# Performance work log

Measured on AMD Instinct MI355X. Metric: run time of the kernel, lower is better.

Reference implementation:

```python
import jax, jax.numpy as jnp
import numpy as np

NEG_SLOPE = 0.2  # PyG GATConv default leaky_relu slope
BN_EPS = 1e-5


def gat_conv(x_src, x_dst, src, dst, w_src, w_dst, att_src, att_dst, bias):
    """Bipartite PyG GATConv, heads=H, concat=False (mean over heads), add_self_loops=True.
    x_src: [Ns, F], x_dst: [Nd, F]; src/dst: [E] int edge index; w_*: [F, H*C]; att_*: [H, C]; bias: [C].
    """
    H, C = att_src.shape
    n_dst = x_dst.shape[0]
    hs = (x_src @ w_src).reshape(-1, H, C)            # [Ns, H, C]
    hd = (x_dst @ w_dst).reshape(-1, H, C)            # [Nd, H, C]
    a_s = (hs * att_src[None]).sum(-1)                # [Ns, H]
    a_d = (hd * att_dst[None]).sum(-1)                # [Nd, H]
    # PyG adds self loops with num_nodes = min(Ns, Nd) for bipartite inputs
    n_loop = min(x_src.shape[0], n_dst)
    loop = jnp.arange(n_loop, dtype=src.dtype)
    src = jnp.concatenate([src, loop])
    dst = jnp.concatenate([dst, loop])
    e = jax.nn.leaky_relu(a_s[src] + a_d[dst], NEG_SLOPE)           # [E+L, H]
    m = jax.ops.segment_max(e, dst, num_segments=n_dst)             # [Nd, H]
    ex = jnp.exp(e - m[dst])
    den = jax.ops.segment_sum(ex, dst, num_segments=n_dst)
    alpha = ex / (den[dst] + 1e-16)                                 # neighborhood softmax
    msg = hs[src] * alpha[:, :, None]                               # [E+L, H, C]
    out = jax.ops.segment_sum(msg, dst, num_segments=n_dst)         # [Nd, H, C]
    return out.mean(axis=1) + bias


def _forward(user_ids, ingredient_ids, recipe_x, ing_src, ing_dst, ub_src, ub_dst,
             user_table, ing_table, W_rl, b_rl, bn_gamma, bn_beta,
             g1_ws, g1_wd, g1_as, g1_ad, g1_b,
             g2_ws, g2_wd, g2_as, g2_ad, g2_b):
    # nn.Embedding(max_norm=1.0): renorm looked-up rows to L2 norm <= 1
    u = user_table[user_ids]
    un = jnp.linalg.norm(u, axis=-1, keepdims=True)
    u = u * jnp.where(un > 1.0, 1.0 / (un + 1e-7), 1.0)
    # static ingredient embedding lookup
    ing = ing_table[ingredient_ids]
    # recipe linear + BatchNorm (training-mode batch stats; dropout off = eval)
    r = recipe_x @ W_rl + b_rl
    mu = r.mean(axis=0)
    var = ((r - mu) ** 2).mean(axis=0)
    r = bn_gamma * (r - mu) * jax.lax.rsqrt(var + BN_EPS) + bn_beta
    # ingredient -> recipe GAT, residual add
    r = r + gat_conv(ing, r, ing_src, ing_dst, g1_ws, g1_wd, g1_as, g1_ad, g1_b)
    # user -> recipe GAT
    r = gat_conv(u, r, ub_src, ub_dst, g2_ws, g2_wd, g2_as, g2_ad, g2_b)
    return r


def setup_inputs() -> dict:
    key = jax.random.key(0)
    ks = jax.random.split(key, 24)
    NU, NR, NI = 50000, 100000, 20000
    D_IN, H, C = 20, 2, 128
    E1, E2 = 400000, 800000
    s = 0.05
    f32 = jnp.float32
    inp = {
        "user_ids": jax.random.randint(ks[0], (NU,), 0, NU, dtype=jnp.int32),
        "ingredient_ids": jax.random.randint(ks[1], (NI,), 0, NI, dtype=jnp.int32),
        "recipe_x": jax.random.normal(ks[2], (NR, D_IN), f32),
        "ing_src": jax.random.randint(ks[3], (E1,), 0, NI, dtype=jnp.int32),
        "ing_dst": jax.random.randint(ks[4], (E1,), 0, NR, dtype=jnp.int32),
        "ub_src": jax.random.randint(ks[5], (E2,), 0, NU, dtype=jnp.int32),
        "ub_dst": jax.random.randint(ks[6], (E2,), 0, NR, dtype=jnp.int32),
        "user_table": jax.random.normal(ks[7], (NU, C), f32) * s,
        "ing_table": jax.random.normal(ks[8], (NI, C), f32) * s,
        "W_rl": jax.random.normal(ks[9], (D_IN, C), f32) * s,
        "b_rl": jnp.zeros((C,), f32),
        "bn_gamma": jnp.ones((C,), f32),
        "bn_beta": jnp.zeros((C,), f32),
        "g1_ws": jax.random.normal(ks[10], (C, H * C), f32) * s,
        "g1_wd": jax.random.normal(ks[11], (C, H * C), f32) * s,
        "g1_as": jax.random.normal(ks[12], (H, C), f32) * s,
        "g1_ad": jax.random.normal(ks[13], (H, C), f32) * s,
        "g1_b": jnp.zeros((C,), f32),
        "g2_ws": jax.random.normal(ks[14], (C, H * C), f32) * s,
        "g2_wd": jax.random.normal(ks[15], (C, H * C), f32) * s,
        "g2_as": jax.random.normal(ks[16], (H, C), f32) * s,
        "g2_ad": jax.random.normal(ks[17], (H, C), f32) * s,
        "g2_b": jnp.zeros((C,), f32),
    }
    return inp


def reference(user_ids, ingredient_ids, recipe_x, ing_src, ing_dst, ub_src, ub_dst,
              user_table, ing_table, W_rl, b_rl, bn_gamma, bn_beta,
              g1_ws, g1_wd, g1_as, g1_ad, g1_b,
              g2_ws, g2_wd, g2_as, g2_ad, g2_b):
    return _forward(user_ids, ingredient_ids, recipe_x, ing_src, ing_dst, ub_src, ub_dst,
                    user_table, ing_table, W_rl, b_rl, bn_gamma, bn_beta,
                    g1_ws, g1_wd, g1_as, g1_ad, g1_b,
                    g2_ws, g2_wd, g2_as, g2_ad, g2_b)
```

## Files before the change

### kernel.cpp

```cpp
#include <hip/hip_runtime.h>
#include <hip/hip_bf16.h>
#include <math.h>

#define DIN 20
#define C 128
#define HC 256
#define EB1 8192
#define EB2 2048
#define MAXNB 400

typedef unsigned short u16;
typedef unsigned int u32;
typedef unsigned long long u64;
typedef __bf16 bf16x8 __attribute__((ext_vector_type(8)));
typedef float f32x4 __attribute__((ext_vector_type(4)));

__device__ __forceinline__ float bfbits2f(unsigned int lo16) {
    return __uint_as_float(lo16 << 16);
}
__device__ __forceinline__ u16 f2bf_rne(float f) {
    unsigned int b = __float_as_uint(f);
    return (u16)((b + 0x7FFFu + ((b >> 16) & 1u)) >> 16);
}

__device__ __forceinline__ void scan512f(u32* cnt, u32* off, u32* wsum4) {
    int t = threadIdx.x;
    int l = t & 63, w = t >> 6;
    u32 a = cnt[2 * t], b = cnt[2 * t + 1];
    u32 s = a + b;
    u32 isc = s;
    #pragma unroll
    for (int o = 1; o < 64; o <<= 1) {
        u32 n = __shfl_up(isc, o);
        if (l >= o) isc += n;
    }
    if (l == 63) wsum4[w] = isc;
    __syncthreads();
    u32 pre = 0;
    if (w > 0) pre += wsum4[0];
    if (w > 1) pre += wsum4[1];
    if (w > 2) pre += wsum4[2];
    u32 excl = pre + isc - s;
    off[2 * t] = excl;
    off[2 * t + 1] = excl + a;
    __syncthreads();
}

__device__ __forceinline__ void edge_at(int i, const int* s1, const int* d1,
    const int* s2, const int* d2, int E1, int T1, int E2, int NR,
    int& s, int& key)
{
    if (i < T1) {
        if (i < E1) { s = s1[i]; key = d1[i]; }
        else        { s = i - E1; key = i - E1; }
    } else {
        int k = i - T1;
        if (k < E2) { s = s2[k]; key = NR + d2[k]; }
        else        { s = k - E2; key = NR + (k - E2); }
    }
}

__global__ __launch_bounds__(256) void k_init(const float* __restrict__ x, int NR,
    float* __restrict__ stats, int SB,
    const int* __restrict__ src1, const int* __restrict__ dst1,
    const int* __restrict__ src2, const int* __restrict__ dst2,
    int E1, int L1, int E2, int L2, int NB, u32* __restrict__ bucketCnt)
{
    __shared__ float L[256][DIN];
    __shared__ u32 cnt[MAXNB];
    int t = threadIdx.x;
    if (blockIdx.x < SB) {
        int r = blockIdx.x * 256 + t;
        if (r < NR) {
            #pragma unroll
            for (int k = 0; k < DIN; k++) L[t][k] = x[r * DIN + k];
        } else {
            #pragma unroll
            for (int k = 0; k < DIN; k++) L[t][k] = 0.f;
        }
        __syncthreads();
        if (t < 210) {
            int p = 0, q = t;
            while (q >= DIN - p) { q -= (DIN - p); p++; }
            q += p;
            float acc = 0.f;
            for (int rr = 0; rr < 256; rr++) acc += L[rr][p] * L[rr][q];
            atomicAdd(&stats[p * DIN + q], acc);
            if (p != q) atomicAdd(&stats[q * DIN + p], acc);
        } else if (t < 230) {
            int k = t - 210;
            float acc = 0.f;
            for (int rr = 0; rr < 256; rr++) acc += L[rr][k];
            atomicAdd(&stats[400 + k], acc);
        }
        return;
    }
    for (int i = t; i < NB; i += 256) cnt[i] = 0;
    __syncthreads();
    int T1 = E1 + L1, T = T1 + E2 + L2;
    int base = (blockIdx.x - SB) * EB1;
    int nE = T - base; if (nE > EB1) nE = EB1;
    for (int j = t; j < nE; j += 256) {
        int s, key;
        edge_at(base + j, src1, dst1, src2, dst2, E1, T1, E2, NR, s, key);
        atomicAdd(&cnt[key >> 9], 1u);
    }
    __syncthreads();
    for (int b = t; b < NB; b += 256) {
        u32 c = cnt[b];
        if (c) atomicAdd(&bucketCnt[b], c);
    }
}

__global__ __launch_bounds__(256) void k_precomp_pack(float* __restrict__ stats,
    const float* __restrict__ W,
    const float* __restrict__ gamma, const float* __restrict__ beta,
    const float* __restrict__ g1_wd, const float* __restrict__ g1_ad,
    const float* __restrict__ g2_wd, const float* __restrict__ g2_ad,
    const float* __restrict__ g1_ws, const float* __restrict__ g1_as,
    const float* __restrict__ g2_ws, const float* __restrict__ g2_as,
    const float* __restrict__ g1b, float invN, u16* __restrict__ wsp,
    const u32* __restrict__ bucketCnt, int NB, int n2,
    u32* __restrict__ bucketBase, u32* __restrict__ gcur, int* __restrict__ off)
{
    int t = threadIdx.x;
    if (blockIdx.x == 33) {
        __shared__ u32 cnt[512], offL[512], wsum4[4];
        for (int i = t; i < 512; i += 256) cnt[i] = (i < NB) ? bucketCnt[i] : 0u;
        __syncthreads();
        scan512f(cnt, offL, wsum4);
        for (int i = t; i < NB; i += 256) {
            u32 v = offL[i];
            bucketBase[i] = v;
            gcur[i] = v;
        }
        if (t == 0) {
            u32 total = offL[511] + cnt[511];
            bucketBase[NB] = total;
            off[n2] = (int)total;
        }
        return;
    }
    if (blockIdx.x > 0) {
        int idx0 = ((blockIdx.x - 1) * 256 + t) * 4;
        #pragma unroll
        for (int i = 0; i < 4; i++) {
            int flat = idx0 + i;
            int j = flat & 7;
            int lane = (flat >> 3) & 63;
            int kb = (flat >> 9) & 3;
            int nt = flat >> 11;
            int k = kb * 32 + (lane >> 4) * 8 + j;
            int n = nt * 16 + (lane & 15);
            wsp[flat] = f2bf_rne(g2_ws[k * HC + n]);
        }
        return;
    }
    __shared__ float Sm[420];
    __shared__ float Wm[DIN * C];
    __shared__ float vd1s[256];
    __shared__ float vd2s[256];
    __shared__ float sS[128];
    __shared__ float sSh[128];
    for (int i = t; i < 420; i += 256) Sm[i] = stats[i];
    for (int i = t; i < DIN * C; i += 256) Wm[i] = W[i];
    __syncthreads();
    if (t < C) {
        float w[DIN];
        #pragma unroll
        for (int k = 0; k < DIN; k++) w[k] = Wm[k * C + t];
        float mb = 0.f;
        #pragma unroll
        for (int k = 0; k < DIN; k++) mb += Sm[400 + k] * invN * w[k];
        float e2 = 0.f;
        for (int p = 0; p < DIN; p++) {
            float acc2 = 0.f;
            #pragma unroll
            for (int q = 0; q < DIN; q++) acc2 += Sm[p * DIN + q] * w[q];
            e2 += w[p] * acc2;
        }
        e2 *= invN;
        float var = e2 - mb * mb;
        float s = gamma[t] * rsqrtf(var + 1e-5f);
        float sh = beta[t] - s * mb;
        stats[420 + t] = s;
        stats[548 + t] = sh;
        sS[t] = s;
        sSh[t] = sh;
    }
    {
        int k = t >> 1, h = t & 1;
        const float4* wd1 = (const float4*)(g1_wd + k * HC + h * C);
        const float4* wd2 = (const float4*)(g2_wd + k * HC + h * C);
        const float4* ws1 = (const float4*)(g1_ws + k * HC + h * C);
        const float4* ws2 = (const float4*)(g2_ws + k * HC + h * C);
        const float4* ad1 = (const float4*)(g1_ad + h * C);
        const float4* ad2 = (const float4*)(g2_ad + h * C);
        const float4* as1 = (const float4*)(g1_as + h * C);
        const float4* as2 = (const float4*)(g2_as + h * C);
        float a1 = 0.f, a2 = 0.f, s1 = 0.f, s2 = 0.f;
        #pragma unroll 4
        for (int q = 0; q < 32; q++) {
            float4 x, y;
            x = wd1[q]; y = ad1[q];
            a1 += x.x * y.x + x.y * y.y + x.z * y.z + x.w * y.w;
            x = wd2[q]; y = ad2[q];
            a2 += x.x * y.x + x.y * y.y + x.z * y.z + x.w * y.w;
            x = ws1[q]; y = as1[q];
            s1 += x.x * y.x + x.y * y.y + x.z * y.z + x.w * y.w;
            x = ws2[q]; y = as2[q];
            s2 += x.x * y.x + x.y * y.y + x.z * y.z + x.w * y.w;
        }
        stats[676 + t] = a1;
        stats[932 + t] = a2;
        stats[1200 + t] = s1;
        stats[1456 + t] = s2;
        vd1s[t] = a1;
        vd2s[t] = a2;
    }
    __syncthreads();
    {
        int k = t >> 1, h = t & 1;
        const float4* ws1p = (const float4*)(g1_ws + k * HC + h * C);
        float t0 = 0.f, t1 = 0.f;
        #pragma unroll 4
        for (int q = 0; q < 32; q++) {
            float4 wv = ws1p[q];
            int c = q * 4;
            t0 += wv.x * vd2s[(c + 0) * 2 + 0] + wv.y * vd2s[(c + 1) * 2 + 0]
                + wv.z * vd2s[(c + 2) * 2 + 0] + wv.w * vd2s[(c + 3) * 2 + 0];
            t1 += wv.x * vd2s[(c + 0) * 2 + 1] + wv.y * vd2s[(c + 1) * 2 + 1]
                + wv.z * vd2s[(c + 2) * 2 + 1] + wv.w * vd2s[(c + 3) * 2 + 1];
        }
        stats[1712 + t * 2 + 0] = t0;
        stats[1712 + t * 2 + 1] = t1;
    }
    if (t < 2) {
        float cb = 0.f;
        for (int k = 0; k < C; k++) cb += g1b[k] * vd2s[k * 2 + t];
        stats[1188 + t] = cb;
    }
    if (t < 80) {
        int k = t >> 2, h4 = t & 3, h = h4 & 1;
        const float* vs = (h4 < 2) ? vd1s : vd2s;
        float acc = 0.f;
        for (int c = 0; c < C; c++) acc += sS[c] * Wm[k * C + c] * vs[c * 2 + h];
        stats[2240 + t] = acc;
    } else if (t < 84) {
        int h4 = t - 80, h = h4 & 1;
        const float* vs = (h4 < 2) ? vd1s : vd2s;
        float acc = 0.f;
        for (int c = 0; c < C; c++) acc += sSh[c] * vs[c * 2 + h];
        stats[2320 + h4] = acc;
    }
}

__global__ __launch_bounds__(256) void k_feat(
    const float* __restrict__ x, int NR, int R0B, int IB,
    const float* __restrict__ ing_table, const int* __restrict__ ing_ids, int NI,
    const float* __restrict__ user_table, const int* __restrict__ user_ids, int NU,
    const u16* __restrict__ wsp, const float* __restrict__ stats,
    float* __restrict__ a_d, float* __restrict__ advd,
    float* __restrict__ a_si, float* __restrict__ psi,
    u16* __restrict__ hs16, float* __restrict__ a_su)
{
    __shared__ float fv[84];
    __shared__ float u1s[256];
    __shared__ float Ts[512];
    __shared__ __align__(16) u16 A[32 * 136];
    __shared__ float u2s[256];
    int t = threadIdx.x;
    int bid = blockIdx.x;
    if (bid < R0B) {
        if (t < 84) fv[t] = stats[2240 + t];
        __syncthreads();
        int r = bid * 256 + t;
        if (r < NR) {
            const float4* xp = (const float4*)(x + (size_t)r * DIN);
            float4 v0 = xp[0], v1 = xp[1], v2 = xp[2], v3 = xp[3], v4 = xp[4];
            float xv[20] = {v0.x, v0.y, v0.z, v0.w, v1.x, v1.y, v1.z, v1.w,
                            v2.x, v2.y, v2.z, v2.w, v3.x, v3.y, v3.z, v3.w,
                            v4.x, v4.y, v4.z, v4.w};
            float a0 = 0.f, a1 = 0.f, b0 = 0.f, b1 = 0.f;
            #pragma unroll
            for (int k = 0; k < DIN; k++) {
                float xvk = xv[k];
                a0 += xvk * fv[k * 4 + 0];
                a1 += xvk * fv[k * 4 + 1];
                b0 += xvk * fv[k * 4 + 2];
                b1 += xvk * fv[k * 4 + 3];
            }
            ((float2*)a_d)[r]  = make_float2(a0 + fv[80], a1 + fv[81]);
            ((float2*)advd)[r] = make_float2(b0 + fv[82], b1 + fv[83]);
        }
        return;
    }
    if (bid < R0B + IB) {
        u1s[t] = stats[1200 + t];
        Ts[t] = stats[1712 + t];
        Ts[256 + t] = stats[1968 + t];
        __syncthreads();
        int r = t >> 3, cg = t & 7;
        int row = (bid - R0B) * 32 + r;
        float as0 = 0.f, as1 = 0.f, p00 = 0.f, p01 = 0.f, p10 = 0.f, p11 = 0.f;
        if (row < NI) {
            const float* xp = ing_table + (size_t)ing_ids[row] * C + cg * 16;
            #pragma unroll
            for (int q = 0; q < 4; q++) {
                float4 v = ((const float4*)xp)[q];
                float xvv[4] = {v.x, v.y, v.z, v.w};
                #pragma unroll
                for (int jj = 0; jj < 4; jj++) {
                    int k = cg * 16 + q * 4 + jj;
                    float xx = xvv[jj];
                    as0 += xx * u1s[k * 2 + 0];
                    as1 += xx * u1s[k * 2 + 1];
                    p00 += xx * Ts[k * 4 + 0];
                    p01 += xx * Ts[k * 4 + 1];
                    p10 += xx * Ts[k * 4 + 2];
                    p11 += xx * Ts[k * 4 + 3];
                }
            }
        }
        #pragma unroll
        for (int m = 1; m <= 4; m <<= 1) {
            as0 += __shfl_xor(as0, m); as1 += __shfl_xor(as1, m);
            p00 += __shfl_xor(p00, m); p01 += __shfl_xor(p01, m);
            p10 += __shfl_xor(p10, m); p11 += __shfl_xor(p11, m);
        }
        if (cg == 0 && row < NI) {
            ((float2*)a_si)[row] = make_float2(as0, as1);
            float4 pv; pv.x = p00; pv.y = p01; pv.z = p10; pv.w = p11;
            ((float4*)psi)[row] = pv;
        }
        return;
    }
    u2s[t] = stats[1456 + t];
    int rowBase = (bid - R0B - IB) * 32;
    int r = t >> 3, cg = t & 7;
    int row = rowBase + r;
    float xv[16];
    if (row < NU) {
        const float* xp = user_table + (size_t)user_ids[row] * C + cg * 16;
        #pragma unroll
        for (int q = 0; q < 4; q++) {
            float4 v = ((const float4*)xp)[q];
            xv[q * 4 + 0] = v.x; xv[q * 4 + 1] = v.y;
            xv[q * 4 + 2] = v.z; xv[q * 4 + 3] = v.w;
        }
    } else {
        #pragma unroll
        for (int q = 0; q < 16; q++) xv[q] = 0.f;
    }
    float ss = 0.f;
    #pragma unroll
    for (int q = 0; q < 16; q++) ss += xv[q] * xv[q];
    #pragma unroll
    for (int m = 1; m <= 4; m <<= 1) ss += __shfl_xor(ss, m);
    float nn = sqrtf(ss);
    float f = (nn > 1.f) ? 1.f / (nn + 1e-7f) : 1.f;
    float as0 = 0.f, as1 = 0.f;
    #pragma unroll
    for (int q = 0; q < 16; q++) {
        xv[q] *= f;
        int k = cg * 16 + q;
        as0 += xv[q] * u2s[k * 2 + 0];
        as1 += xv[q] * u2s[k * 2 + 1];
    }
    #pragma unroll
    for (int m = 1; m <= 4; m <<= 1) {
        as0 += __shfl_xor(as0, m); as1 += __shfl_xor(as1, m);
    }
    if (cg == 0 && row < NU) ((float2*)a_su)[row] = make_float2(as0, as1);
    {
        union { u16 h[16]; uint4 u4[2]; } pk;
        #pragma unroll
        for (int q = 0; q < 16; q++) pk.h[q] = f2bf_rne(xv[q]);
        uint4* dst = (uint4*)&A[r * 136 + cg * 16];
        dst[0] = pk.u4[0];
        dst[1] = pk.u4[1];
    }
    __syncthreads();
    int w = t >> 6, l = t & 63;
    int m15 = l & 15, q4 = l >> 4;
    bf16x8 afrag[2][4];
    #pragma unroll
    for (int mt = 0; mt < 2; mt++)
        #pragma unroll
        for (int kb = 0; kb < 4; kb++)
            afrag[mt][kb] = *(const bf16x8*)&A[(mt * 16 + m15) * 136 + kb * 32 + q4 * 8];
    f32x4 acc[2][4];
    #pragma unroll
    for (int mt = 0; mt < 2; mt++)
        #pragma unroll
        for (int i = 0; i < 4; i++) acc[mt][i] = (f32x4){0.f, 0.f, 0.f, 0.f};
    #pragma unroll
    for (int kb = 0; kb < 4; kb++) {
        #pragma unroll
        for (int i = 0; i < 4; i++) {
            int nt = w * 4 + i;
            bf16x8 bfrag = *(const bf16x8*)&wsp[((nt * 4 + kb) * 64 + l) * 8];
            acc[0][i] = __builtin_amdgcn_mfma_f32_16x16x32_bf16(afrag[0][kb], bfrag, acc[0][i], 0, 0, 0);
            acc[1][i] = __builtin_amdgcn_mfma_f32_16x16x32_bf16(afrag[1][kb], bfrag, acc[1][i], 0, 0, 0);
        }
    }
    #pragma unroll
    for (int mt = 0; mt < 2; mt++) {
        #pragma unroll
        for (int i = 0; i < 4; i++) {
            int col = (w * 4 + i) * 16 + m15;
            #pragma unroll
            for (int rr = 0; rr < 4; rr++) {
                int rw = rowBase + mt * 16 + q4 * 4 + rr;
                if (rw < NU) hs16[(size_t)rw * HC + col] = f2bf_rne(acc[mt][i][rr]);
            }
        }
    }
}

__global__ __launch_bounds__(256) void kA2(const int* __restrict__ src1, const int* __restrict__ dst1,
    const int* __restrict__ src2, const int* __restrict__ dst2,
    int E1, int L1, int E2, int L2, int NR, int NB,
    u32* __restrict__ gcur, u64* __restrict__ pairs)
{
    __shared__ u64 ldsE[EB2];
    __shared__ u64 ldsS[EB2];
    __shared__ u32 cntA[512], cntB[512], offL[512], wsum4[4];
    __shared__ u32 gbase[MAXNB];
    int t = threadIdx.x;
    for (int i = t; i < 512; i += 256) { cntA[i] = 0; cntB[i] = 0; }
    __syncthreads();
    int T1 = E1 + L1, T = T1 + E2 + L2;
    int base = blockIdx.x * EB2;
    int nE = T - base; if (nE > EB2) nE = EB2;
    for (int j = t; j < nE; j += 256) {
        int s, key;
        edge_at(base + j, src1, dst1, src2, dst2, E1, T1, E2, NR, s, key);
        ldsE[j] = ((u64)(u32)key << 32) | (u32)s;
        atomicAdd(&cntA[key >> 9], 1u);
    }
    __syncthreads();
    scan512f(cntA, offL, wsum4);
    for (int b = t; b < NB; b += 256) {
        u32 c = cntA[b];
        gbase[b] = c ? atomicAdd(&gcur[b], c) : 0u;
    }
    __syncthreads();
    for (int j = t; j < nE; j += 256) {
        u64 e = ldsE[j];
        u32 b = ((u32)(e >> 32)) >> 9;
        u32 r = atomicAdd(&cntB[b], 1u);
        ldsS[offL[b] + r] = e;
    }
    __syncthreads();
    for (int j = t; j < nE; j += 256) {
        u64 e = ldsS[j];
        u32 b = ((u32)(e >> 32)) >> 9;
        pairs[gbase[b] + ((u32)j - offL[b])] = e;
    }
}

__global__ __launch_bounds__(256) void kB(const u64* __restrict__ pairs,
    const u32* __restrict__ bucketBase, int n2,
    int* __restrict__ off, int* __restrict__ sorted)
{
    __shared__ u32 cntA[512], cntB[512], offL[512], wsum4[4];
    __shared__ u32 ldsS[8192];
    int b = blockIdx.x;
    int t = threadIdx.x;
    u32 beg = bucketBase[b], end = bucketBase[b + 1];
    int dstBase = b << 9;
    for (int i = t; i < 512; i += 256) { cntA[i] = 0; cntB[i] = 0; }
    __syncthreads();
    for (u32 j = beg + t; j < end; j += 256) {
        u32 key = (u32)(pairs[j] >> 32);
        atomicAdd(&cntA[key - dstBase], 1u);
    }
    __syncthreads();
    scan512f(cntA, offL, wsum4);
    for (int d = t; d < 512; d += 256) {
        int gk = dstBase + d;
        if (gk < n2) off[gk] = (int)(beg + offL[d]);
    }
    u32 cnt = end - beg;
    bool fast = cnt <= 8192u;
    __syncthreads();
    for (u32 j = beg + t; j < end; j += 256) {
        u64 e = pairs[j];
        u32 d = (u32)(e >> 32) - dstBase;
        u32 r = atomicAdd(&cntB[d], 1u);
        u32 pos = offL[d] + r;
        if (fast) ldsS[pos] = (u32)e;
        else sorted[beg + pos] = (int)(u32)e;
    }
    __syncthreads();
    if (fast) {
        for (u32 j = t; j < cnt; j += 256) sorted[beg + j] = (int)ldsS[j];
    }
}

__global__ __launch_bounds__(256) void k_agg(const int* __restrict__ off, const int* __restrict__ sorted,
    const float* __restrict__ a_si, const float* __restrict__ psi,
    const float* __restrict__ a_d1, const float* __restrict__ advd,
    const float* __restrict__ cb,
    const float* __restrict__ a_su, const u16* __restrict__ hs16,
    const float* __restrict__ bias, int NR, float* __restrict__ out)
{
    int wave = threadIdx.x >> 6, lane = threadIdx.x & 63;
    int d = blockIdx.x * 4 + wave;
    if (d >= NR) return;
    int beg = off[d], end = off[d + 1];
    float ad0 = a_d1[d * 2 + 0], ad1 = a_d1[d * 2 + 1];
    float w0s = 0.f, w1s = 0.f, a00 = 0.f, a01 = 0.f, a10 = 0.f, a11 = 0.f;
    for (int j = beg + lane; j < end; j += 64) {
        int s = sorted[j];
        float2 as = ((const float2*)a_si)[s];
        float e0 = as.x + ad0; e0 = (e0 >= 0.f) ? e0 : 0.2f * e0;
        float e1 = as.y + ad1; e1 = (e1 >= 0.f) ? e1 : 0.2f * e1;
        float x0 = __expf(e0), x1 = __expf(e1);
        float4 p = ((const float4*)psi)[s];
        w0s += x0; w1s += x1;
        a00 += x0 * p.x; a01 += x0 * p.y;
        a10 += x1 * p.z; a11 += x1 * p.w;
    }
    #pragma unroll
    for (int o = 1; o < 64; o <<= 1) {
        w0s += __shfl_xor(w0s, o); w1s += __shfl_xor(w1s, o);
        a00 += __shfl_xor(a00, o); a01 += __shfl_xor(a01, o);
        a10 += __shfl_xor(a10, o); a11 += __shfl_xor(a11, o);
    }
    float inv0g = 1.f / (w0s + 1e-16f), inv1g = 1.f / (w1s + 1e-16f);
    float r0 = advd[d * 2 + 0] + cb[0] + 0.5f * (a00 * inv0g + a10 * inv1g);
    float r1 = advd[d * 2 + 1] + cb[1] + 0.5f * (a01 * inv0g + a11 * inv1g);
    int beg2 = off[NR + d], end2 = off[NR + d + 1];
    int head = lane >> 5;
    int q = lane & 31;
    u32 laneoff = (u32)(head * 256 + q * 8);
    int hsel = lane & 32;
    float adh = head ? r1 : r0;
    float wsum = 0.f;
    float acc0 = 0.f, acc1 = 0.f, acc2 = 0.f, acc3 = 0.f;
    const char* hbase = (const char*)hs16;

    for (int base = beg2; base < end2; base += 32) {
        int rem = end2 - base; if (rem > 32) rem = 32;
        int j = q; if (j >= rem) j = rem - 1;
        int sp = sorted[base + j];
        u32 boff = ((u32)sp) << 9;
        float asv = a_su[sp * 2 + head];
        float ee = asv + adh; ee = (ee >= 0.f) ? ee : 0.2f * ee;
        float wcomb = __expf(ee);
        int e = 0;
        for (; e + 4 <= rem; e += 4) {
            u32 b0 = __shfl(boff, e + 0), b1 = __shfl(boff, e + 1);
            u32 b2 = __shfl(boff, e + 2), b3 = __shfl(boff, e + 3);
            uint2 g0 = *(const uint2*)(hbase + (b0 + laneoff));
            uint2 g1 = *(const uint2*)(hbase + (b1 + laneoff));
            uint2 g2 = *(const uint2*)(hbase + (b2 + laneoff));
            uint2 g3 = *(const uint2*)(hbase + (b3 + laneoff));
            float W0 = __shfl(wcomb, hsel + e + 0);
            float W1 = __shfl(wcomb, hsel + e + 1);
            float W2 = __shfl(wcomb, hsel + e + 2);
            float W3 = __shfl(wcomb, hsel + e + 3);
            wsum += (W0 + W1) + (W2 + W3);
            acc0 += W0 * bfbits2f(g0.x & 0xFFFFu);
            acc1 += W0 * __uint_as_float(g0.x & 0xFFFF0000u);
            acc2 += W0 * bfbits2f(g0.y & 0xFFFFu);
            acc3 += W0 * __uint_as_float(g0.y & 0xFFFF0000u);
            acc0 += W1 * bfbits2f(g1.x & 0xFFFFu);
            acc1 += W1 * __uint_as_float(g1.x & 0xFFFF0000u);
            acc2 += W1 * bfbits2f(g1.y & 0xFFFFu);
            acc3 += W1 * __uint_as_float(g1.y & 0xFFFF0000u);
            acc0 += W2 * bfbits2f(g2.x & 0xFFFFu);
            acc1 += W2 * __uint_as_float(g2.x & 0xFFFF0000u);
            acc2 += W2 * bfbits2f(g2.y & 0xFFFFu);
            acc3 += W2 * __uint_as_float(g2.y & 0xFFFF0000u);
            acc0 += W3 * bfbits2f(g3.x & 0xFFFFu);
            acc1 += W3 * __uint_as_float(g3.x & 0xFFFF0000u);
            acc2 += W3 * bfbits2f(g3.y & 0xFFFFu);
            acc3 += W3 * __uint_as_float(g3.y & 0xFFFF0000u);
        }
        for (; e < rem; e++) {
            u32 b0 = __shfl(boff, e);
            float W = __shfl(wcomb, hsel + e);
            uint2 g = *(const uint2*)(hbase + (b0 + laneoff));
            wsum += W;
            acc0 += W * bfbits2f(g.x & 0xFFFFu);
            acc1 += W * __uint_as_float(g.x & 0xFFFF0000u);
            acc2 += W * bfbits2f(g.y & 0xFFFFu);
            acc3 += W * __uint_as_float(g.y & 0xFFFF0000u);
        }
    }
    float inv = 1.f / (wsum + 1e-16f);
    float v0 = acc0 * inv, v1 = acc1 * inv, v2 = acc2 * inv, v3 = acc3 * inv;
    v0 = 0.5f * (v0 + __shfl_xor(v0, 32));
    v1 = 0.5f * (v1 + __shfl_xor(v1, 32));
    v2 = 0.5f * (v2 + __shfl_xor(v2, 32));
    v3 = 0.5f * (v3 + __shfl_xor(v3, 32));
    if (lane < 32) {
        float4 bb = ((const float4*)bias)[q];
        float4 o;
        o.x = v0 + bb.x; o.y = v1 + bb.y; o.z = v2 + bb.z; o.w = v3 + bb.w;
        ((float4*)(out + (size_t)d * C))[q] = o;
    }
}

extern "C" void kernel_launch(void* const* d_in, const int* in_sizes, int n_in,
                              void* d_out, int out_size, void* d_ws, size_t ws_size,
                              hipStream_t stream) {
    const int*   user_ids       = (const int*)d_in[0];
    const int*   ingredient_ids = (const int*)d_in[1];
    const float* recipe_x       = (const float*)d_in[2];
    const int*   ing_src        = (const int*)d_in[3];
    const int*   ing_dst        = (const int*)d_in[4];
    const int*   ub_src         = (const int*)d_in[5];
    const int*   ub_dst         = (const int*)d_in[6];
    const float* user_table     = (const float*)d_in[7];
    const float* ing_table      = (const float*)d_in[8];
    const float* W_rl           = (const float*)d_in[9];
    const float* bn_gamma       = (const float*)d_in[11];
    const float* bn_beta        = (const float*)d_in[12];
    const float* g1_ws          = (const float*)d_in[13];
    const float* g1_wd          = (const float*)d_in[14];
    const float* g1_as          = (const float*)d_in[15];
    const float* g1_ad          = (const float*)d_in[16];
    const float* g1_b           = (const float*)d_in[17];
    const float* g2_ws          = (const float*)d_in[18];
    const float* g2_wd          = (const float*)d_in[19];
    const float* g2_as          = (const float*)d_in[20];
    const float* g2_ad          = (const float*)d_in[21];
    const float* g2_b           = (const float*)d_in[22];

    int NU = in_sizes[0];
    int NI = in_sizes[1];
    int NR = in_sizes[2] / DIN;
    int E1 = in_sizes[3];
    int E2 = in_sizes[5];
    int Nmax = (NI > NU) ? NI : NU;
    int L1 = (NI < NR) ? NI : NR;
    int L2 = (NU < NR) ? NU : NR;
    int Etot = E1 + L1 + E2 + L2;
    int n2 = 2 * NR;
    int NB = (n2 + 511) >> 9;

    char* w = (char*)d_ws;
    u16*   hs16  = (u16*)w;    w += (size_t)Nmax * HC * 2;
    float* a_si  = (float*)w;  w += (size_t)NI * 2 * 4;
    float* a_su  = (float*)w;  w += (size_t)NU * 2 * 4;
    float* psi   = (float*)w;  w += (size_t)NI * 4 * 4;
    float* a_d   = (float*)w;  w += (size_t)NR * 2 * 4;
    float* advd  = (float*)w;  w += (size_t)NR * 2 * 4;
    float* stats = (float*)w;  w += 2432 * 4;
    u32*   bucketCnt  = (u32*)w; w += MAXNB * 4;
    u16*   wsp   = (u16*)w;    w += 32768 * 2;
    u32*   bucketBase = (u32*)w; w += (MAXNB + 1) * 4;
    u32*   gcur  = (u32*)w;    w += MAXNB * 4;
    int*   off   = (int*)w;    w += (size_t)(n2 + 1) * 4;
    int*   sorted= (int*)w;    w += (size_t)Etot * 4;
    w = (char*)(((size_t)w + 15) & ~(size_t)15);
    u64*   pairs = (u64*)w;    w += (size_t)Etot * 8;

    hipMemsetAsync(stats, 0, (2432 + MAXNB) * 4, stream);

    int SB = (NR + 255) / 256;
    int AB = (Etot + EB1 - 1) / EB1;
    k_init<<<SB + AB, 256, 0, stream>>>(recipe_x, NR, stats, SB,
                                        ing_src, ing_dst, ub_src, ub_dst,
                                        E1, L1, E2, L2, NB, bucketCnt);
    k_precomp_pack<<<34, 256, 0, stream>>>(stats, W_rl, bn_gamma, bn_beta,
                                           g1_wd, g1_ad, g2_wd, g2_ad,
                                           g1_ws, g1_as, g2_ws, g2_as, g1_b,
                                           1.0f / NR, wsp,
                                           bucketCnt, NB, n2, bucketBase, gcur, off);
    kA2<<<(Etot + EB2 - 1) / EB2, 256, 0, stream>>>(ing_src, ing_dst, ub_src, ub_dst,
                                                    E1, L1, E2, L2, NR, NB, gcur, pairs);
    int R0B = (NR + 255) / 256;
    int IB  = (NI + 31) / 32;
    int HB  = (NU + 31) / 32;
    k_feat<<<R0B + IB + HB, 256, 0, stream>>>(recipe_x, NR, R0B, IB,
                                              ing_table, ingredient_ids, NI,
                                              user_table, user_ids, NU,
                                              wsp, stats, a_d, advd, a_si, psi,
                                              hs16, a_su);
    kB<<<NB, 256, 0, stream>>>(pairs, bucketBase, n2, off, sorted);
    k_agg<<<(NR + 3) / 4, 256, 0, stream>>>(off, sorted, a_si, psi, a_d, advd,
                                            stats + 1188, a_su, hs16, g2_b, NR,
                                            (float*)d_out);
}
```

Baseline: 352.4 us.

## Merge bucket-sort and feature kernels into fewer launches with shared LDS

Folds the bf16 weight packing into k_init and the edge scatter (kA2) into the feature kernel as k_mid. It also merges the per-bucket sort (kB) with the user GEMM blocks as k_fin, cutting the launch count from six to five. Independent work now runs concurrently inside one grid. To make the merged kernels fit, the scatter chunk EB2 is halved and the LDS fast-path threshold in the bucket sort drops from 8192 to 6144. That sends more buckets down the slower global-scatter path and doubles the number of scatter blocks and global atomics on gcur.

```diff
diff --git a/kernel.cpp b/kernel.cpp
--- a/kernel.cpp
+++ b/kernel.cpp
@@ -6,7 +6,7 @@
 #define C 128
 #define HC 256
 #define EB1 8192
-#define EB2 2048
+#define EB2 1024
 #define MAXNB 400
 
 typedef unsigned short u16;
@@ -61,16 +61,17 @@
 }
 
 __global__ __launch_bounds__(256) void k_init(const float* __restrict__ x, int NR,
-    float* __restrict__ stats, int SB,
-    const int* __restrict__ src1, const int* __restrict__ dst1,
-    const int* __restrict__ src2, const int* __restrict__ dst2,
-    int E1, int L1, int E2, int L2, int NB, u32* __restrict__ bucketCnt)
+    float* __restrict__ stats, int SB, int AB,
+    const int* __restrict__ dst1, const int* __restrict__ dst2,
+    int E1, int L1, int E2, int L2, int NB, u32* __restrict__ bucketCnt,
+    const float* __restrict__ g2_ws, u16* __restrict__ wsp)
 {
     __shared__ float L[256][DIN];
     __shared__ u32 cnt[MAXNB];
     int t = threadIdx.x;
-    if (blockIdx.x < SB) {
-        int r = blockIdx.x * 256 + t;
+    int bid = blockIdx.x;
+    if (bid < SB) {
+        int r = bid * 256 + t;
         if (r < NR) {
             #pragma unroll
             for (int k = 0; k < DIN; k++) L[t][k] = x[r * DIN + k];
@@ -95,36 +96,52 @@
         }
         return;
     }
-    for (int i = t; i < NB; i += 256) cnt[i] = 0;
-    __syncthreads();
-    int T1 = E1 + L1, T = T1 + E2 + L2;
-    int base = (blockIdx.x - SB) * EB1;
-    int nE = T - base; if (nE > EB1) nE = EB1;
-    for (int j = t; j < nE; j += 256) {
-        int s, key;
-        edge_at(base + j, src1, dst1, src2, dst2, E1, T1, E2, NR, s, key);
-        atomicAdd(&cnt[key >> 9], 1u);
-    }
-    __syncthreads();
-    for (int b = t; b < NB; b += 256) {
-        u32 c = cnt[b];
-        if (c) atomicAdd(&bucketCnt[b], c);
-    }
-}
-
-__global__ __launch_bounds__(256) void k_precomp_pack(float* __restrict__ stats,
+    if (bid < SB + AB) {
+        for (int i = t; i < NB; i += 256) cnt[i] = 0;
+        __syncthreads();
+        int T1 = E1 + L1, T = T1 + E2 + L2;
+        int base = (bid - SB) * EB1;
+        int nE = T - base; if (nE > EB1) nE = EB1;
+        for (int j = t; j < nE; j += 256) {
+            int i = base + j, key;
+            if (i < T1) key = (i < E1) ? dst1[i] : (i - E1);
+            else { int k = i - T1; key = NR + ((k < E2) ? dst2[k] : (k - E2)); }
+            atomicAdd(&cnt[key >> 9], 1u);
+        }
+        __syncthreads();
+        for (int b = t; b < NB; b += 256) {
+            u32 c = cnt[b];
+            if (c) atomicAdd(&bucketCnt[b], c);
+        }
+        return;
+    }
+    int idx0 = ((bid - SB - AB) * 256 + t) * 4;
+    #pragma unroll
+    for (int i = 0; i < 4; i++) {
+        int flat = idx0 + i;
+        int j = flat & 7;
+        int lane = (flat >> 3) & 63;
+        int kb = (flat >> 9) & 3;
+        int nt = flat >> 11;
+        int k = kb * 32 + (lane >> 4) * 8 + j;
+        int n = nt * 16 + (lane & 15);
+        wsp[flat] = f2bf_rne(g2_ws[k * HC + n]);
+    }
+}
+
+__global__ __launch_bounds__(256) void k_scanpre(float* __restrict__ stats,
     const float* __restrict__ W,
     const float* __restrict__ gamma, const float* __restrict__ beta,
     const float* __restrict__ g1_wd, const float* __restrict__ g1_ad,
     const float* __restrict__ g2_wd, const float* __restrict__ g2_ad,
     const float* __restrict__ g1_ws, const float* __restrict__ g1_as,
     const float* __restrict__ g2_ws, const float* __restrict__ g2_as,
-    const float* __restrict__ g1b, float invN, u16* __restrict__ wsp,
+    const float* __restrict__ g1b, float invN,
     const u32* __restrict__ bucketCnt, int NB, int n2,
     u32* __restrict__ bucketBase, u32* __restrict__ gcur, int* __restrict__ off)
 {
     int t = threadIdx.x;
-    if (blockIdx.x == 33) {
+    if (blockIdx.x == 1) {
         __shared__ u32 cnt[512], offL[512], wsum4[4];
         for (int i = t; i < 512; i += 256) cnt[i] = (i < NB) ? bucketCnt[i] : 0u;
         __syncthreads();
@@ -138,21 +155,6 @@
             u32 total = offL[511] + cnt[511];
             bucketBase[NB] = total;
             off[n2] = (int)total;
-        }
-        return;
-    }
-    if (blockIdx.x > 0) {
-        int idx0 = ((blockIdx.x - 1) * 256 + t) * 4;
-        #pragma unroll
-        for (int i = 0; i < 4; i++) {
-            int flat = idx0 + i;
-            int j = flat & 7;
-            int lane = (flat >> 3) & 63;
-            int kb = (flat >> 9) & 3;
-            int nt = flat >> 11;
-            int k = kb * 32 + (lane >> 4) * 8 + j;
-            int n = nt * 16 + (lane & 15);
-            wsp[flat] = f2bf_rne(g2_ws[k * HC + n]);
         }
         return;
     }
@@ -255,26 +257,64 @@
     }
 }
 
-__global__ __launch_bounds__(256) void k_feat(
-    const float* __restrict__ x, int NR, int R0B, int IB,
+__global__ __launch_bounds__(256) void k_mid(
+    const int* __restrict__ src1, const int* __restrict__ dst1,
+    const int* __restrict__ src2, const int* __restrict__ dst2,
+    int E1, int L1, int E2, int L2, int NR, int NB,
+    u32* __restrict__ gcur, u64* __restrict__ pairs, int A2B, int R0B,
+    const float* __restrict__ x, const float* __restrict__ stats,
+    float* __restrict__ a_d, float* __restrict__ advd,
     const float* __restrict__ ing_table, const int* __restrict__ ing_ids, int NI,
-    const float* __restrict__ user_table, const int* __restrict__ user_ids, int NU,
-    const u16* __restrict__ wsp, const float* __restrict__ stats,
-    float* __restrict__ a_d, float* __restrict__ advd,
-    float* __restrict__ a_si, float* __restrict__ psi,
-    u16* __restrict__ hs16, float* __restrict__ a_su)
+    float* __restrict__ a_si, float* __restrict__ psi)
 {
-    __shared__ float fv[84];
-    __shared__ float u1s[256];
-    __shared__ float Ts[512];
-    __shared__ __align__(16) u16 A[32 * 136];
-    __shared__ float u2s[256];
+    __shared__ __align__(16) char sm[24144];
     int t = threadIdx.x;
     int bid = blockIdx.x;
-    if (bid < R0B) {
+    if (bid < A2B) {
+        u64* ldsE = (u64*)sm;
+        u64* ldsS = ldsE + EB2;
+        u32* cntA = (u32*)(ldsS + EB2);
+        u32* cntB = cntA + 512;
+        u32* offL = cntB + 512;
+        u32* wsum4 = offL + 512;
+        u32* gbase = wsum4 + 4;
+        for (int i = t; i < 512; i += 256) { cntA[i] = 0; cntB[i] = 0; }
+        __syncthreads();
+        int T1 = E1 + L1, T = T1 + E2 + L2;
+        int base = bid * EB2;
+        int nE = T - base; if (nE > EB2) nE = EB2;
+        for (int j = t; j < nE; j += 256) {
+            int s, key;
+            edge_at(base + j, src1, dst1, src2, dst2, E1, T1, E2, NR, s, key);
+            ldsE[j] = ((u64)(u32)key << 32) | (u32)s;
+            atomicAdd(&cntA[key >> 9], 1u);
+        }
+        __syncthreads();
+        scan512f(cntA, offL, wsum4);
+        for (int b = t; b < NB; b += 256) {
+            u32 c = cntA[b];
+            gbase[b] = c ? atomicAdd(&gcur[b], c) : 0u;
+        }
+        __syncthreads();
+        for (int j = t; j < nE; j += 256) {
+            u64 e = ldsE[j];
+            u32 b = ((u32)(e >> 32)) >> 9;
+            u32 r = atomicAdd(&cntB[b], 1u);
+            ldsS[offL[b] + r] = e;
+        }
+        __syncthreads();
+        for (int j = t; j < nE; j += 256) {
+            u64 e = ldsS[j];
+            u32 b = ((u32)(e >> 32)) >> 9;
+            pairs[gbase[b] + ((u32)j - offL[b])] = e;
+        }
+        return;
+    }
+    if (bid < A2B + R0B) {
+        float* fv = (float*)sm;
         if (t < 84) fv[t] = stats[2240 + t];
         __syncthreads();
-        int r = bid * 256 + t;
+        int r = (bid - A2B) * 256 + t;
         if (r < NR) {
             const float4* xp = (const float4*)(x + (size_t)r * DIN);
             float4 v0 = xp[0], v1 = xp[1], v2 = xp[2], v3 = xp[3], v4 = xp[4];
@@ -295,48 +335,99 @@
         }
         return;
     }
-    if (bid < R0B + IB) {
-        u1s[t] = stats[1200 + t];
-        Ts[t] = stats[1712 + t];
-        Ts[256 + t] = stats[1968 + t];
-        __syncthreads();
-        int r = t >> 3, cg = t & 7;
-        int row = (bid - R0B) * 32 + r;
-        float as0 = 0.f, as1 = 0.f, p00 = 0.f, p01 = 0.f, p10 = 0.f, p11 = 0.f;
-        if (row < NI) {
-            const float* xp = ing_table + (size_t)ing_ids[row] * C + cg * 16;
+    float* u1s = (float*)sm;
+    float* Ts  = u1s + 256;
+    u1s[t] = stats[1200 + t];
+    Ts[t] = stats[1712 + t];
+    Ts[256 + t] = stats[1968 + t];
+    __syncthreads();
+    int r = t >> 3, cg = t & 7;
+    int row = (bid - A2B - R0B) * 32 + r;
+    float as0 = 0.f, as1 = 0.f, p00 = 0.f, p01 = 0.f, p10 = 0.f, p11 = 0.f;
+    if (row < NI) {
+        const float* xp = ing_table + (size_t)ing_ids[row] * C + cg * 16;
+        #pragma unroll
+        for (int q = 0; q < 4; q++) {
+            float4 v = ((const float4*)xp)[q];
+            float xvv[4] = {v.x, v.y, v.z, v.w};
             #pragma unroll
-            for (int q = 0; q < 4; q++) {
-                float4 v = ((const float4*)xp)[q];
-                float xvv[4] = {v.x, v.y, v.z, v.w};
-                #pragma unroll
-                for (int jj = 0; jj < 4; jj++) {
-                    int k = cg * 16 + q * 4 + jj;
-                    float xx = xvv[jj];
-                    as0 += xx * u1s[k * 2 + 0];
-                    as1 += xx * u1s[k * 2 + 1];
-                    p00 += xx * Ts[k * 4 + 0];
-                    p01 += xx * Ts[k * 4 + 1];
-                    p10 += xx * Ts[k * 4 + 2];
-                    p11 += xx * Ts[k * 4 + 3];
-                }
+            for (int jj = 0; jj < 4; jj++) {
+                int k = cg * 16 + q * 4 + jj;
+                float xx = xvv[jj];
+                as0 += xx * u1s[k * 2 + 0];
+                as1 += xx * u1s[k * 2 + 1];
+                p00 += xx * Ts[k * 4 + 0];
+                p01 += xx * Ts[k * 4 + 1];
+                p10 += xx * Ts[k * 4 + 2];
+                p11 += xx * Ts[k * 4 + 3];
             }
         }
-        #pragma unroll
-        for (int m = 1; m <= 4; m <<= 1) {
-            as0 += __shfl_xor(as0, m); as1 += __shfl_xor(as1, m);
-            p00 += __shfl_xor(p00, m); p01 += __shfl_xor(p01, m);
-            p10 += __shfl_xor(p10, m); p11 += __shfl_xor(p11, m);
-        }
-        if (cg == 0 && row < NI) {
-            ((float2*)a_si)[row] = make_float2(as0, as1);
-            float4 pv; pv.x = p00; pv.y = p01; pv.z = p10; pv.w = p11;
-            ((float4*)psi)[row] = pv;
+    }
+    #pragma unroll
+    for (int m = 1; m <= 4; m <<= 1) {
+        as0 += __shfl_xor(as0, m); as1 += __shfl_xor(as1, m);
+        p00 += __shfl_xor(p00, m); p01 += __shfl_xor(p01, m);
+        p10 += __shfl_xor(p10, m); p11 += __shfl_xor(p11, m);
+    }
+    if (cg == 0 && row < NI) {
+        ((float2*)a_si)[row] = make_float2(as0, as1);
+        float4 pv; pv.x = p00; pv.y = p01; pv.z = p10; pv.w = p11;
+        ((float4*)psi)[row] = pv;
+    }
+}
+
+__global__ __launch_bounds__(256) void k_fin(const u64* __restrict__ pairs,
+    const u32* __restrict__ bucketBase, int n2, int NB,
+    int* __restrict__ off, int* __restrict__ sorted,
+    const float* __restrict__ user_table, const int* __restrict__ user_ids, int NU,
+    const u16* __restrict__ wsp, const float* __restrict__ stats,
+    u16* __restrict__ hs16, float* __restrict__ a_su)
+{
+    __shared__ __align__(16) char sm[30736];
+    int t = threadIdx.x;
+    int bid = blockIdx.x;
+    if (bid < NB) {
+        u32* cntA = (u32*)sm;
+        u32* cntB = cntA + 512;
+        u32* offL = cntB + 512;
+        u32* wsum4 = offL + 512;
+        u32* ldsS = wsum4 + 4;
+        int b = bid;
+        u32 beg = bucketBase[b], end = bucketBase[b + 1];
+        int dstBase = b << 9;
+        for (int i = t; i < 512; i += 256) { cntA[i] = 0; cntB[i] = 0; }
+        __syncthreads();
+        for (u32 j = beg + t; j < end; j += 256) {
+            u32 key = (u32)(pairs[j] >> 32);
+            atomicAdd(&cntA[key - dstBase], 1u);
+        }
+        __syncthreads();
+        scan512f(cntA, offL, wsum4);
+        for (int d = t; d < 512; d += 256) {
+            int gk = dstBase + d;
+            if (gk < n2) off[gk] = (int)(beg + offL[d]);
+        }
+        u32 cnt = end - beg;
+        bool fast = cnt <= 6144u;
+        __syncthreads();
+        for (u32 j = beg + t; j < end; j += 256) {
+            u64 e = pairs[j];
+            u32 d = (u32)(e >> 32) - dstBase;
+            u32 r = atomicAdd(&cntB[d], 1u);
+            u32 pos = offL[d] + r;
+            if (fast) ldsS[pos] = (u32)e;
+            else sorted[beg + pos] = (int)(u32)e;
+        }
+        __syncthreads();
+        if (fast) {
+            for (u32 j = t; j < cnt; j += 256) sorted[beg + j] = (int)ldsS[j];
         }
         return;
     }
+    u16* A = (u16*)sm;
+    float* u2s = (float*)(sm + 8704);
     u2s[t] = stats[1456 + t];
-    int rowBase = (bid - R0B - IB) * 32;
+    int rowBase = (bid - NB) * 32;
     int r = t >> 3, cg = t & 7;
     int row = rowBase + r;
     float xv[16];
@@ -415,87 +506,6 @@
                 if (rw < NU) hs16[(size_t)rw * HC + col] = f2bf_rne(acc[mt][i][rr]);
             }
         }
-    }
-}
-
-__global__ __launch_bounds__(256) void kA2(const int* __restrict__ src1, const int* __restrict__ dst1,
-    const int* __restrict__ src2, const int* __restrict__ dst2,
-    int E1, int L1, int E2, int L2, int NR, int NB,
-    u32* __restrict__ gcur, u64* __restrict__ pairs)
-{
-    __shared__ u64 ldsE[EB2];
-    __shared__ u64 ldsS[EB2];
-    __shared__ u32 cntA[512], cntB[512], offL[512], wsum4[4];
-    __shared__ u32 gbase[MAXNB];
-    int t = threadIdx.x;
-    for (int i = t; i < 512; i += 256) { cntA[i] = 0; cntB[i] = 0; }
-    __syncthreads();
-    int T1 = E1 + L1, T = T1 + E2 + L2;
-    int base = blockIdx.x * EB2;
-    int nE = T - base; if (nE > EB2) nE = EB2;
-    for (int j = t; j < nE; j += 256) {
-        int s, key;
-        edge_at(base + j, src1, dst1, src2, dst2, E1, T1, E2, NR, s, key);
-        ldsE[j] = ((u64)(u32)key << 32) | (u32)s;
-        atomicAdd(&cntA[key >> 9], 1u);
-    }
-    __syncthreads();
-    scan512f(cntA, offL, wsum4);
-    for (int b = t; b < NB; b += 256) {
-        u32 c = cntA[b];
-        gbase[b] = c ? atomicAdd(&gcur[b], c) : 0u;
-    }
-    __syncthreads();
-    for (int j = t; j < nE; j += 256) {
-        u64 e = ldsE[j];
-        u32 b = ((u32)(e >> 32)) >> 9;
-        u32 r = atomicAdd(&cntB[b], 1u);
-        ldsS[offL[b] + r] = e;
-    }
-    __syncthreads();
-    for (int j = t; j < nE; j += 256) {
-        u64 e = ldsS[j];
-        u32 b = ((u32)(e >> 32)) >> 9;
-        pairs[gbase[b] + ((u32)j - offL[b])] = e;
-    }
-}
-
-__global__ __launch_bounds__(256) void kB(const u64* __restrict__ pairs,
-    const u32* __restrict__ bucketBase, int n2,
-    int* __restrict__ off, int* __restrict__ sorted)
-{
-    __shared__ u32 cntA[512], cntB[512], offL[512], wsum4[4];
-    __shared__ u32 ldsS[8192];
-    int b = blockIdx.x;
-    int t = threadIdx.x;
-    u32 beg = bucketBase[b], end = bucketBase[b + 1];
-    int dstBase = b << 9;
-    for (int i = t; i < 512; i += 256) { cntA[i] = 0; cntB[i] = 0; }
-    __syncthreads();
-    for (u32 j = beg + t; j < end; j += 256) {
-        u32 key = (u32)(pairs[j] >> 32);
-        atomicAdd(&cntA[key - dstBase], 1u);
-    }
-    __syncthreads();
-    scan512f(cntA, offL, wsum4);
-    for (int d = t; d < 512; d += 256) {
-        int gk = dstBase + d;
-        if (gk < n2) off[gk] = (int)(beg + offL[d]);
-    }
-    u32 cnt = end - beg;
-    bool fast = cnt <= 8192u;
-    __syncthreads();
-    for (u32 j = beg + t; j < end; j += 256) {
-        u64 e = pairs[j];
-        u32 d = (u32)(e >> 32) - dstBase;
-        u32 r = atomicAdd(&cntB[d], 1u);
-        u32 pos = offL[d] + r;
-        if (fast) ldsS[pos] = (u32)e;
-        else sorted[beg + pos] = (int)(u32)e;
-    }
-    __syncthreads();
-    if (fast) {
-        for (u32 j = t; j < cnt; j += 256) sorted[beg + j] = (int)ldsS[j];
     }
 }
 
@@ -664,25 +674,25 @@
 
     int SB = (NR + 255) / 256;
     int AB = (Etot + EB1 - 1) / EB1;
-    k_init<<<SB + AB, 256, 0, stream>>>(recipe_x, NR, stats, SB,
-                                        ing_src, ing_dst, ub_src, ub_dst,
-                                        E1, L1, E2, L2, NB, bucketCnt);
-    k_precomp_pack<<<34, 256, 0, stream>>>(stats, W_rl, bn_gamma, bn_beta,
-                                           g1_wd, g1_ad, g2_wd, g2_ad,
-                                           g1_ws, g1_as, g2_ws, g2_as, g1_b,
-                                           1.0f / NR, wsp,
-                                           bucketCnt, NB, n2, bucketBase, gcur, off);
-    kA2<<<(Etot + EB2 - 1) / EB2, 256, 0, stream>>>(ing_src, ing_dst, ub_src, ub_dst,
-                                                    E1, L1, E2, L2, NR, NB, gcur, pairs);
+    k_init<<<SB + AB + 32, 256, 0, stream>>>(recipe_x, NR, stats, SB, AB,
+                                             ing_dst, ub_dst, E1, L1, E2, L2, NB,
+                                             bucketCnt, g2_ws, wsp);
+    k_scanpre<<<2, 256, 0, stream>>>(stats, W_rl, bn_gamma, bn_beta,
+                                     g1_wd, g1_ad, g2_wd, g2_ad,
+                                     g1_ws, g1_as, g2_ws, g2_as, g1_b,
+                                     1.0f / NR,
+                                     bucketCnt, NB, n2, bucketBase, gcur, off);
+    int A2B = (Etot + EB2 - 1) / EB2;
     int R0B = (NR + 255) / 256;
     int IB  = (NI + 31) / 32;
-    int HB  = (NU + 31) / 32;
-    k_feat<<<R0B + IB + HB, 256, 0, stream>>>(recipe_x, NR, R0B, IB,
-                                              ing_table, ingredient_ids, NI,
-                                              user_table, user_ids, NU,
-                                              wsp, stats, a_d, advd, a_si, psi,
-                                              hs16, a_su);
-    kB<<<NB, 256, 0, stream>>>(pairs, bucketBase, n2, off, sorted);
+    k_mid<<<A2B + R0B + IB, 256, 0, stream>>>(ing_src, ing_dst, ub_src, ub_dst,
+                                              E1, L1, E2, L2, NR, NB, gcur, pairs,
+                                              A2B, R0B, recipe_x, stats, a_d, advd,
+                                              ing_table, ingredient_ids, NI, a_si, psi);
+    int HB = (NU + 31) / 32;
+    k_fin<<<NB + HB, 256, 0, stream>>>(pairs, bucketBase, n2, NB, off, sorted,
+                                       user_table, user_ids, NU, wsp, stats,
+                                       hs16, a_su);
     k_agg<<<(NR + 3) / 4, 256, 0, stream>>>(off, sorted, a_si, psi, a_d, advd,
                                             stats + 1188, a_su, hs16, g2_b, NR,
                                             (float*)d_out);
```

After: 359.1 us. About the same (+1.9%).
